# Optimization experiments

Measured on AMD Instinct MI355X. Metric: run time of the kernel, lower is better.

The kernel has to match this reference:

```python
import jax, jax.numpy as jnp
import numpy as np

N = 100_000   # nodes
E = 1_200_000 # edges
D = 64        # in_dim
H = 64        # hidden_dim
B = 1000      # graphs in batch
C = 10        # num_classes
TOPO = 64     # topo_dim
BN_EPS = 1e-5


def setup_inputs() -> dict:
    key = jax.random.key(0)
    ks = jax.random.split(key, 24)
    x = jax.random.normal(ks[0], (N, D), dtype=jnp.float32)
    edge_index = jax.random.randint(ks[1], (2, E), 0, N, dtype=jnp.int32)
    # sorted graph ids; force last id = B-1 so batch.max()+1 == B (matches torch path)
    batch = jnp.sort(jax.random.randint(ks[2], (N,), 0, B, dtype=jnp.int32)).at[-1].set(B - 1)
    topo = jax.random.normal(ks[3], (B, TOPO), dtype=jnp.float32)
    s = 0.05
    return {
        "x": x, "edge_index": edge_index, "batch": batch, "topo": topo,
        # conv1 MLP: Linear(D,H) -> BN(H) -> ReLU -> Linear(H,H) -> ReLU
        "W1a": jax.random.normal(ks[4], (D, H)) * s, "b1a": jax.random.normal(ks[5], (H,)) * s,
        "g1": 1.0 + jax.random.normal(ks[6], (H,)) * s, "be1": jax.random.normal(ks[7], (H,)) * s,
        "m1": jax.random.normal(ks[8], (H,)) * s, "v1": 0.5 + jax.random.uniform(ks[9], (H,)),
        "W1b": jax.random.normal(ks[10], (H, H)) * s, "b1b": jax.random.normal(ks[11], (H,)) * s,
        # conv2 MLP: Linear(H,H) -> BN(H) -> ReLU
        "W2": jax.random.normal(ks[12], (H, H)) * s, "b2": jax.random.normal(ks[13], (H,)) * s,
        "g2": 1.0 + jax.random.normal(ks[14], (H,)) * s, "be2": jax.random.normal(ks[15], (H,)) * s,
        "m2": jax.random.normal(ks[16], (H,)) * s, "v2": 0.5 + jax.random.uniform(ks[17], (H,)),
        # topo_net: Linear(TOPO,H) -> ReLU
        "Wt": jax.random.normal(ks[18], (TOPO, H)) * s, "bt": jax.random.normal(ks[19], (H,)) * s,
        # classifier: Linear(2H, C)
        "Wc": jax.random.normal(ks[20], (2 * H, C)) * s, "bc": jax.random.normal(ks[21], (C,)) * s,
    }


def _bn_eval(v, g, b, m, var):
    # BatchNorm1d in eval mode: affine with running stats
    return g * (v - m) * jax.lax.rsqrt(var + BN_EPS) + b


def _gin_agg(h, src, dst):
    # GINConv (eps=0): (1+eps)*x_i + sum_{j->i} x_j ; scatter-add over dst
    return h + jax.ops.segment_sum(h[src], dst, num_segments=N)


def reference(x, edge_index, batch, topo,
              W1a, b1a, g1, be1, m1, v1, W1b, b1b,
              W2, b2, g2, be2, m2, v2, Wt, bt, Wc, bc):
    src, dst = edge_index[0], edge_index[1]
    # conv1: MLP(agg(x)) = Lin -> BN -> ReLU -> Lin -> ReLU; outer relu from forward
    h = _gin_agg(x, src, dst)                              # [N, D]
    h = jax.nn.relu(_bn_eval(h @ W1a + b1a, g1, be1, m1, v1))
    h = jax.nn.relu(h @ W1b + b1b)                         # [N, H]
    h = jax.nn.relu(h)                                     # F.relu(conv1(...))
    # dropout(p=0.5) is identity in eval mode
    # conv2: Lin -> BN -> ReLU, then outer relu
    h = _gin_agg(h, src, dst)                              # [N, H]
    h = jax.nn.relu(_bn_eval(h @ W2 + b2, g2, be2, m2, v2))
    h = jax.nn.relu(h)
    # global_add_pool: sum nodes per graph
    x_struct = jax.ops.segment_sum(h, batch, num_segments=B)   # [B, H]
    # topo already [B, TOPO] => all reshape/pad branches are no-ops
    x_topo = jax.nn.relu(topo @ Wt + bt)                   # [B, H]
    combined = jnp.concatenate([x_struct, x_topo], axis=1) # [B, 2H]
    return combined @ Wc + bc                              # [B, C]
```

## Files before the change

### kernel.cpp

```cpp
#include <hip/hip_runtime.h>

#define N_NODES 100000
#define N_EDGES 1200000
#define DIM     64
#define BGRAPHS 1000
#define NCLASS  10
#define BN_EPS  1e-5f

#define NBUCK   256
#define NPB     391
#define MAGIC   10984572u
#define CHUNK   8192
#define NBLK_P  147
#define CAP     8192
#define NB_C    3125

typedef __attribute__((ext_vector_type(8))) short   bfx8;
typedef __attribute__((ext_vector_type(4))) float   f32x4;
typedef __attribute__((ext_vector_type(8))) unsigned short u16x8;

__device__ __forceinline__ unsigned short f2bf(float f) {
    unsigned u = __builtin_bit_cast(unsigned, f);
    unsigned r = (u + 0x7FFFu + ((u >> 16) & 1u)) >> 16;
    return (unsigned short)r;
}
__device__ __forceinline__ float bf2f(unsigned short h) {
    unsigned u = ((unsigned)h) << 16;
    return __builtin_bit_cast(float, u);
}

__global__ __launch_bounds__(256) void convhist_kernel(
    const float* __restrict__ x, unsigned short* __restrict__ xb,
    float* __restrict__ xs, const int* __restrict__ ei,
    int* __restrict__ gpart,
    const float* __restrict__ W1a, const float* __restrict__ W1b,
    const float* __restrict__ W2,
    unsigned short* __restrict__ w1ap, unsigned short* __restrict__ w1bp,
    unsigned short* __restrict__ w2p) {
    __shared__ int cnt[NBUCK];
    int t = threadIdx.x;
    if (blockIdx.x < NBLK_P) {
        int blk = blockIdx.x;
        cnt[t] = 0;
        __syncthreads();
        int e0 = blk * CHUNK;
        for (int i = t; i < CHUNK; i += 256) {
            int e = e0 + i;
            if (e >= N_EDGES) break;
            unsigned d = (unsigned)ei[N_EDGES + e];
            atomicAdd(&cnt[__umulhi(d, MAGIC)], 1);
        }
        __syncthreads();
        gpart[blk * NBUCK + t] = cnt[t];
    } else if (blockIdx.x < NBLK_P + NB_C) {
        int i = (blockIdx.x - NBLK_P) * 256 + t;
        const int n8 = N_NODES * DIM / 8;
        if (i < n8) {
            float4 a = ((const float4*)x)[i * 2];
            float4 b = ((const float4*)x)[i * 2 + 1];
            u16x8 o;
            o[0] = f2bf(a.x); o[1] = f2bf(a.y); o[2] = f2bf(a.z); o[3] = f2bf(a.w);
            o[4] = f2bf(b.x); o[5] = f2bf(b.y); o[6] = f2bf(b.z); o[7] = f2bf(b.w);
            ((u16x8*)xb)[i] = o;
        }
        if (i < BGRAPHS * DIM) xs[i] = 0.f;
    } else {
        const float* Ws[3] = {W1a, W1b, W2};
        unsigned short* Wp[3] = {w1ap, w1bp, w2p};
        #pragma unroll
        for (int wsel = 0; wsel < 3; ++wsel) {
            const float* W = Ws[wsel];
            #pragma unroll
            for (int r = 0; r < 2; ++r) {
                int e = r * 256 + t;
                int kt = e >> 8, q = (e >> 6) & 3, col = e & 63;
                u16x8 o;
                #pragma unroll
                for (int j = 0; j < 8; ++j)
                    o[j] = f2bf(W[(kt * 32 + q * 8 + j) * 64 + col]);
                ((u16x8*)Wp[wsel])[e] = o;
            }
        }
    }
}

__global__ __launch_bounds__(256) void scanB_kernel(const int* __restrict__ gpart,
                                                    int* __restrict__ base,
                                                    int* __restrict__ cursor) {
    __shared__ int tmp[256];
    int t = threadIdx.x;
    int s = 0;
    for (int blk = 0; blk < NBLK_P; ++blk) s += gpart[blk * NBUCK + t];
    tmp[t] = s;
    __syncthreads();
    for (int off = 1; off < 256; off <<= 1) {
        int a = (t >= off) ? tmp[t - off] : 0;
        __syncthreads();
        tmp[t] += a;
        __syncthreads();
    }
    int excl = tmp[t] - s;
    base[t] = excl;
    cursor[t] = excl;
    if (t == 255) base[256] = N_EDGES;
}

__global__ __launch_bounds__(256) void part_kernel(const int* __restrict__ ei,
                                                   int* __restrict__ cursor,
                                                   int* __restrict__ srcbuf,
                                                   unsigned short* __restrict__ dstlbuf) {
    __shared__ int cnt[NBUCK];
    __shared__ int cur[NBUCK];
    int t = threadIdx.x, blk = blockIdx.x;
    cnt[t] = 0;
    __syncthreads();
    int e0 = blk * CHUNK;
    for (int i = t; i < CHUNK; i += 256) {
        int e = e0 + i;
        if (e >= N_EDGES) break;
        unsigned d = (unsigned)ei[N_EDGES + e];
        atomicAdd(&cnt[__umulhi(d, MAGIC)], 1);
    }
    __syncthreads();
    cur[t] = atomicAdd(&cursor[t], cnt[t]);
    __syncthreads();
    for (int i = t; i < CHUNK; i += 256) {
        int e = e0 + i;
        if (e >= N_EDGES) break;
        unsigned d = (unsigned)ei[N_EDGES + e];
        int s = ei[e];
        int b = __umulhi(d, MAGIC);
        int pos = atomicAdd(&cur[b], 1);
        srcbuf[pos] = s;
        dstlbuf[pos] = (unsigned short)(d - b * NPB);
    }
}

__global__ __launch_bounds__(256) void refine_kernel(const int* __restrict__ srcbuf,
                                                     const unsigned short* __restrict__ dstlbuf,
                                                     const int* __restrict__ base,
                                                     int* __restrict__ csr_src,
                                                     int* __restrict__ rowptr) {
    __shared__ int cnt[NPB + 1];
    __shared__ int cur[NPB + 1];
    __shared__ int tmp[256];
    __shared__ int outb[CAP];
    int t = threadIdx.x, b = blockIdx.x;
    int beg = base[b];
    int end = base[b + 1];

    for (int i = t; i < NPB + 1; i += 256) cnt[i] = 0;
    __syncthreads();
    for (int i = beg + t; i < end; i += 256)
        atomicAdd(&cnt[dstlbuf[i]], 1);
    __syncthreads();

    int i0 = 2 * t, i1 = 2 * t + 1;
    int v0 = (i0 < NPB) ? cnt[i0] : 0;
    int v1 = (i1 < NPB) ? cnt[i1] : 0;
    int s = v0 + v1;
    tmp[t] = s;
    __syncthreads();
    for (int off = 1; off < 256; off <<= 1) {
        int a = (t >= off) ? tmp[t - off] : 0;
        __syncthreads();
        tmp[t] += a;
        __syncthreads();
    }
    int excl = tmp[t] - s;
    if (i0 < NPB) cur[i0] = excl;
    if (i1 < NPB) cur[i1] = excl + v0;
    {
        int g0 = b * NPB + i0;
        if (i0 < NPB && g0 < N_NODES) rowptr[g0] = beg + excl;
        int g1 = b * NPB + i1;
        if (i1 < NPB && g1 < N_NODES) rowptr[g1] = beg + excl + v0;
    }
    if (b == NBUCK - 1 && t == 0) rowptr[N_NODES] = N_EDGES;
    __syncthreads();

    for (int i = beg + t; i < end; i += 256) {
        int dl = dstlbuf[i];
        int pos = atomicAdd(&cur[dl], 1);
        if (pos < CAP) outb[pos] = srcbuf[i];
    }
    __syncthreads();

    int nb = end - beg; if (nb > CAP) nb = CAP;
    for (int i = t; i < nb; i += 256) csr_src[beg + i] = outb[i];
}

__global__ __launch_bounds__(256) void gather_kernel(const unsigned short* __restrict__ feat,
                                                     const int* __restrict__ rowptr,
                                                     const int* __restrict__ csr_src,
                                                     unsigned short* __restrict__ out) {
    int t = threadIdx.x;
    int node = blockIdx.x * 32 + (t >> 3);
    int q = t & 7;
    if (node >= N_NODES) return;
    const u16x8* f8 = (const u16x8*)feat;
    u16x8 sv = f8[(long long)node * 8 + q];
    float acc[8];
    #pragma unroll
    for (int j = 0; j < 8; ++j) acc[j] = bf2f(sv[j]);
    int beg = rowptr[node], end = rowptr[node + 1];
    int k = beg;
    int sn = (k < end) ? csr_src[k] : 0;
    while (k < end) {
        int sc = sn;
        ++k;
        if (k < end) sn = csr_src[k];
        u16x8 v = f8[(long long)sc * 8 + q];
        #pragma unroll
        for (int j = 0; j < 8; ++j) acc[j] += bf2f(v[j]);
    }
    u16x8 o;
    #pragma unroll
    for (int j = 0; j < 8; ++j) o[j] = f2bf(acc[j]);
    ((u16x8*)out)[(long long)node * 8 + q] = o;
}

__global__ __launch_bounds__(256) void mlp1_kernel(
    const unsigned short* __restrict__ h0,
    const unsigned short* __restrict__ w1ap, const float* __restrict__ b1a,
    const float* __restrict__ g1,  const float* __restrict__ be1,
    const float* __restrict__ m1,  const float* __restrict__ v1,
    const unsigned short* __restrict__ w1bp, const float* __restrict__ b1b,
    unsigned short* __restrict__ h2) {
    __shared__ unsigned short h1t[4][16 * 72];
    __shared__ unsigned short outt[4][16 * 64];

    int t = threadIdx.x;
    int w = t >> 6, lane = t & 63;
    int m = lane & 15, q = lane >> 4;
    int row0 = blockIdx.x * 64 + w * 16;

    const bfx8* wap = (const bfx8*)w1ap;
    const bfx8* wbp = (const bfx8*)w1bp;
    bfx8 wa[4][2], wb[4][2];
    #pragma unroll
    for (int nt = 0; nt < 4; ++nt) {
        #pragma unroll
        for (int kt = 0; kt < 2; ++kt) {
            int idx = (kt * 4 + q) * 64 + nt * 16 + m;
            wa[nt][kt] = wap[idx];
            wb[nt][kt] = wbp[idx];
        }
    }
    float A1[4], B1[4], B2c[4];
    #pragma unroll
    for (int nt = 0; nt < 4; ++nt) {
        int c = nt * 16 + m;
        float s = g1[c] * rsqrtf(v1[c] + BN_EPS);
        A1[nt] = s;
        B1[nt] = b1a[c] * s + (be1[c] - m1[c] * s);
        B2c[nt] = b1b[c];
    }

    int rowA = row0 + m;
    if (rowA > N_NODES - 1) rowA = N_NODES - 1;
    const bfx8* ap = (const bfx8*)(h0 + (long long)rowA * 64);
    bfx8 a0 = ap[q];
    bfx8 a1 = ap[4 + q];
    f32x4 acc[4];
    #pragma unroll
    for (int nt = 0; nt < 4; ++nt) {
        acc[nt] = (f32x4){0.f, 0.f, 0.f, 0.f};
        acc[nt] = __builtin_amdgcn_mfma_f32_16x16x32_bf16(a0, wa[nt][0], acc[nt], 0, 0, 0);
        acc[nt] = __builtin_amdgcn_mfma_f32_16x16x32_bf16(a1, wa[nt][1], acc[nt], 0, 0, 0);
    }
    #pragma unroll
    for (int nt = 0; nt < 4; ++nt)
        #pragma unroll
        for (int r = 0; r < 4; ++r) {
            float v = fmaxf(acc[nt][r] * A1[nt] + B1[nt], 0.f);
            h1t[w][(q * 4 + r) * 72 + nt * 16 + m] = f2bf(v);
        }
    __syncthreads();

    const bfx8* hp = (const bfx8*)&h1t[w][m * 72];
    bfx8 c0 = hp[q];
    bfx8 c1 = hp[4 + q];
    f32x4 acc2[4];
    #pragma unroll
    for (int nt = 0; nt < 4; ++nt) {
        acc2[nt] = (f32x4){0.f, 0.f, 0.f, 0.f};
        acc2[nt] = __builtin_amdgcn_mfma_f32_16x16x32_bf16(c0, wb[nt][0], acc2[nt], 0, 0, 0);
        acc2[nt] = __builtin_amdgcn_mfma_f32_16x16x32_bf16(c1, wb[nt][1], acc2[nt], 0, 0, 0);
    }
    #pragma unroll
    for (int nt = 0; nt < 4; ++nt)
        #pragma unroll
        for (int r = 0; r < 4; ++r) {
            float v = fmaxf(acc2[nt][r] + B2c[nt], 0.f);
            outt[w][(q * 4 + r) * 64 + nt * 16 + m] = f2bf(v);
        }
    __syncthreads();

    #pragma unroll
    for (int i = lane; i < 128; i += 64) {
        int rr = i >> 3, cc = i & 7;
        int rg = row0 + rr;
        if (rg < N_NODES)
            ((float4*)h2)[(long long)rg * 8 + cc] = *(const float4*)&outt[w][rr * 64 + cc * 8];
    }
}

__global__ __launch_bounds__(256) void mlp2_kernel(
    const unsigned short* __restrict__ h3,
    const unsigned short* __restrict__ w2p, const float* __restrict__ b2,
    const float* __restrict__ g2, const float* __restrict__ be2,
    const float* __restrict__ m2, const float* __restrict__ v2,
    const int* __restrict__ batch,
    float* __restrict__ xs) {
    __shared__ float pool[64 * 64];
    __shared__ int bts[64];

    int t = threadIdx.x;
    int w = t >> 6, lane = t & 63;
    int m = lane & 15, q = lane >> 4;
    int row0b = blockIdx.x * 64;
    int row0 = row0b + w * 16;

    const bfx8* wpp = (const bfx8*)w2p;
    bfx8 wf[4][2];
    #pragma unroll
    for (int nt = 0; nt < 4; ++nt)
        #pragma unroll
        for (int kt = 0; kt < 2; ++kt)
            wf[nt][kt] = wpp[(kt * 4 + q) * 64 + nt * 16 + m];
    float A[4], Bc[4];
    #pragma unroll
    for (int nt = 0; nt < 4; ++nt) {
        int c = nt * 16 + m;
        float s = g2[c] * rsqrtf(v2[c] + BN_EPS);
        A[nt] = s;
        Bc[nt] = b2[c] * s + (be2[c] - m2[c] * s);
    }
    if (t < 64) {
        int rg = row0b + t;
        bts[t] = (rg < N_NODES) ? batch[rg] : -1;
    }

    int rowA = row0 + m;
    if (rowA > N_NODES - 1) rowA = N_NODES - 1;
    const bfx8* ap = (const bfx8*)(h3 + (long long)rowA * 64);
    bfx8 a0 = ap[q];
    bfx8 a1 = ap[4 + q];
    f32x4 acc[4];
    #pragma unroll
    for (int nt = 0; nt < 4; ++nt) {
        acc[nt] = (f32x4){0.f, 0.f, 0.f, 0.f};
        acc[nt] = __builtin_amdgcn_mfma_f32_16x16x32_bf16(a0, wf[nt][0], acc[nt], 0, 0, 0);
        acc[nt] = __builtin_amdgcn_mfma_f32_16x16x32_bf16(a1, wf[nt][1], acc[nt], 0, 0, 0);
    }
    #pragma unroll
    for (int nt = 0; nt < 4; ++nt)
        #pragma unroll
        for (int r = 0; r < 4; ++r) {
            float v = fmaxf(acc[nt][r] * A[nt] + Bc[nt], 0.f);
            pool[(w * 16 + q * 4 + r) * 64 + nt * 16 + m] = v;
        }
    __syncthreads();

    int col = t & 63;
    int r0 = (t >> 6) * 16;
    int cb = bts[r0];
    float cur = 0.f;
    #pragma unroll
    for (int r = 0; r < 16; ++r) {
        int b = bts[r0 + r];
        if (b != cb) {
            if (cb >= 0) unsafeAtomicAdd(&xs[cb * 64 + col], cur);
            cb = b;
            cur = 0.f;
        }
        cur += pool[(r0 + r) * 64 + col];
    }
    if (cb >= 0) unsafeAtomicAdd(&xs[cb * 64 + col], cur);
}

__global__ __launch_bounds__(64) void head_kernel(
    const float* __restrict__ xs, const float* __restrict__ topo,
    const float* __restrict__ Wt, const float* __restrict__ bt,
    const float* __restrict__ Wc, const float* __restrict__ bc,
    float* __restrict__ out) {
    __shared__ float trow[64];
    __shared__ float comb[128];
    int b = blockIdx.x;
    int h = threadIdx.x;
    trow[h] = topo[b * 64 + h];
    __syncthreads();
    float acc = bt[h];
    #pragma unroll
    for (int k = 0; k < 64; ++k) acc += trow[k] * Wt[k * 64 + h];
    comb[h] = xs[b * 64 + h];
    comb[64 + h] = fmaxf(acc, 0.f);
    __syncthreads();
    if (h < NCLASS) {
        float o = bc[h];
        #pragma unroll
        for (int k = 0; k < 128; ++k) o += comb[k] * Wc[k * NCLASS + h];
        out[b * NCLASS + h] = o;
    }
}

extern "C" void kernel_launch(void* const* d_in, const int* in_sizes, int n_in,
                              void* d_out, int out_size, void* d_ws, size_t ws_size,
                              hipStream_t stream) {
    const float* x     = (const float*)d_in[0];
    const int*   ei    = (const int*)d_in[1];
    const int*   batch = (const int*)d_in[2];
    const float* topo  = (const float*)d_in[3];
    const float* W1a   = (const float*)d_in[4];
    const float* b1a   = (const float*)d_in[5];
    const float* g1    = (const float*)d_in[6];
    const float* be1   = (const float*)d_in[7];
    const float* m1    = (const float*)d_in[8];
    const float* v1    = (const float*)d_in[9];
    const float* W1b   = (const float*)d_in[10];
    const float* b1b   = (const float*)d_in[11];
    const float* W2    = (const float*)d_in[12];
    const float* b2    = (const float*)d_in[13];
    const float* g2    = (const float*)d_in[14];
    const float* be2   = (const float*)d_in[15];
    const float* m2    = (const float*)d_in[16];
    const float* v2    = (const float*)d_in[17];
    const float* Wt    = (const float*)d_in[18];
    const float* bt    = (const float*)d_in[19];
    const float* Wc    = (const float*)d_in[20];
    const float* bc    = (const float*)d_in[21];
    float* out = (float*)d_out;

    char* p = (char*)d_ws;
    unsigned short* xbf  = (unsigned short*)p; p += (size_t)N_NODES * DIM * 2;
    unsigned short* bufA = (unsigned short*)p; p += (size_t)N_NODES * DIM * 2;
    unsigned short* bufB = (unsigned short*)p; p += (size_t)N_NODES * DIM * 2;
    float* xs      = (float*)p; p += (size_t)BGRAPHS * DIM * 4;
    int*   rowptr  = (int*)p;   p += (size_t)(N_NODES + 16) * 4;
    int*   gpart   = (int*)p;   p += (size_t)NBLK_P * NBUCK * 4;
    int*   base    = (int*)p;   p += 1040;
    int*   cursor  = (int*)p;   p += 1024;
    unsigned short* w1ap = (unsigned short*)p; p += 512 * 16;
    unsigned short* w1bp = (unsigned short*)p; p += 512 * 16;
    unsigned short* w2p  = (unsigned short*)p; p += 512 * 16;
    int*   srcbuf  = (int*)p;   p += (size_t)N_EDGES * 4;
    unsigned short* dstlbuf = (unsigned short*)p; p += (size_t)N_EDGES * 2;
    int*   csr_src = (int*)p;

    convhist_kernel<<<NBLK_P + NB_C + 1, 256, 0, stream>>>(
        x, xbf, xs, ei, gpart, W1a, W1b, W2, w1ap, w1bp, w2p);
    scanB_kernel<<<1, 256, 0, stream>>>(gpart, base, cursor);
    part_kernel<<<NBLK_P, 256, 0, stream>>>(ei, cursor, srcbuf, dstlbuf);
    refine_kernel<<<NBUCK, 256, 0, stream>>>(srcbuf, dstlbuf, base, csr_src, rowptr);
    gather_kernel<<<(N_NODES + 31) / 32, 256, 0, stream>>>(xbf, rowptr, csr_src, bufA);
    mlp1_kernel<<<(N_NODES + 63) / 64, 256, 0, stream>>>(
        bufA, w1ap, b1a, g1, be1, m1, v1, w1bp, b1b, bufB);
    gather_kernel<<<(N_NODES + 31) / 32, 256, 0, stream>>>(bufB, rowptr, csr_src, bufA);
    mlp2_kernel<<<(N_NODES + 63) / 64, 256, 0, stream>>>(
        bufA, w2p, b2, g2, be2, m2, v2, batch, xs);
    head_kernel<<<BGRAPHS, 64, 0, stream>>>(xs, topo, Wt, bt, Wc, bc, out);
}
```

Baseline: 246.9 us.

## Apply linear layers before aggregation and fuse BN/ReLU and pooling into gathers

Uses linearity of the GIN sum: x@W1a is computed in the prep kernel before aggregation, and h@W2 in the mid MLP, so the gather kernels run on projected features and apply the folded BN affine plus ReLU in their epilogue. The second gather also does the global add pool directly, which removes the separate mlp2 kernel and one full feature round-trip. BN scale and shift are precomputed once into a small buffer, and part_kernel reuses the histogram counts instead of recounting. Rounding changes because the projection is rounded to bf16 before summation, and the guards for node counts that are not a multiple of 32 are dropped.

```diff
diff --git a/kernel.cpp b/kernel.cpp
--- a/kernel.cpp
+++ b/kernel.cpp
@@ -13,7 +13,7 @@
 #define CHUNK   8192
 #define NBLK_P  147
 #define CAP     8192
-#define NB_C    3125
+#define NB_G    1563
 
 typedef __attribute__((ext_vector_type(8))) short   bfx8;
 typedef __attribute__((ext_vector_type(4))) float   f32x4;
@@ -29,15 +29,30 @@
     return __builtin_bit_cast(float, u);
 }
 
-__global__ __launch_bounds__(256) void convhist_kernel(
-    const float* __restrict__ x, unsigned short* __restrict__ xb,
-    float* __restrict__ xs, const int* __restrict__ ei,
+__device__ __forceinline__ bfx8 load_wfrag(const float* __restrict__ W, int kt, int q, int col) {
+    bfx8 f;
+    #pragma unroll
+    for (int j = 0; j < 8; ++j)
+        f[j] = (short)f2bf(W[(kt * 32 + q * 8 + j) * 64 + col]);
+    return f;
+}
+
+__global__ __launch_bounds__(256) void prep_kernel(
+    const float* __restrict__ x, const int* __restrict__ ei,
     int* __restrict__ gpart,
-    const float* __restrict__ W1a, const float* __restrict__ W1b,
-    const float* __restrict__ W2,
-    unsigned short* __restrict__ w1ap, unsigned short* __restrict__ w1bp,
-    unsigned short* __restrict__ w2p) {
+    const float* __restrict__ W1a, unsigned short* __restrict__ y0,
+    float* __restrict__ xs,
+    const float* __restrict__ W1b, const float* __restrict__ W2,
+    unsigned short* __restrict__ w1bp, unsigned short* __restrict__ w2p,
+    const float* __restrict__ b1a, const float* __restrict__ g1,
+    const float* __restrict__ be1, const float* __restrict__ m1,
+    const float* __restrict__ v1,
+    const float* __restrict__ b2,  const float* __restrict__ g2,
+    const float* __restrict__ be2, const float* __restrict__ m2,
+    const float* __restrict__ v2,
+    float* __restrict__ AB) {
     __shared__ int cnt[NBUCK];
+    __shared__ unsigned short outt[4][16 * 64];
     int t = threadIdx.x;
     if (blockIdx.x < NBLK_P) {
         int blk = blockIdx.x;
@@ -52,23 +67,54 @@
         }
         __syncthreads();
         gpart[blk * NBUCK + t] = cnt[t];
-    } else if (blockIdx.x < NBLK_P + NB_C) {
-        int i = (blockIdx.x - NBLK_P) * 256 + t;
-        const int n8 = N_NODES * DIM / 8;
-        if (i < n8) {
-            float4 a = ((const float4*)x)[i * 2];
-            float4 b = ((const float4*)x)[i * 2 + 1];
-            u16x8 o;
-            o[0] = f2bf(a.x); o[1] = f2bf(a.y); o[2] = f2bf(a.z); o[3] = f2bf(a.w);
-            o[4] = f2bf(b.x); o[5] = f2bf(b.y); o[6] = f2bf(b.z); o[7] = f2bf(b.w);
-            ((u16x8*)xb)[i] = o;
-        }
-        if (i < BGRAPHS * DIM) xs[i] = 0.f;
+    } else if (blockIdx.x < NBLK_P + NB_G) {
+        int g = blockIdx.x - NBLK_P;
+        if (g < (BGRAPHS * DIM) / 256) xs[g * 256 + t] = 0.f;
+        int w = t >> 6, lane = t & 63;
+        int m = lane & 15, q = lane >> 4;
+        int row0 = g * 64 + w * 16;
+
+        bfx8 wa[4][2];
+        #pragma unroll
+        for (int nt = 0; nt < 4; ++nt)
+            #pragma unroll
+            for (int kt = 0; kt < 2; ++kt)
+                wa[nt][kt] = load_wfrag(W1a, kt, q, nt * 16 + m);
+
+        int rowA = row0 + m;
+        if (rowA > N_NODES - 1) rowA = N_NODES - 1;
+        const float* xp = x + (long long)rowA * 64;
+        bfx8 a0, a1;
+        #pragma unroll
+        for (int j = 0; j < 8; ++j) {
+            a0[j] = (short)f2bf(xp[q * 8 + j]);
+            a1[j] = (short)f2bf(xp[32 + q * 8 + j]);
+        }
+        f32x4 acc[4];
+        #pragma unroll
+        for (int nt = 0; nt < 4; ++nt) {
+            acc[nt] = (f32x4){0.f, 0.f, 0.f, 0.f};
+            acc[nt] = __builtin_amdgcn_mfma_f32_16x16x32_bf16(a0, wa[nt][0], acc[nt], 0, 0, 0);
+            acc[nt] = __builtin_amdgcn_mfma_f32_16x16x32_bf16(a1, wa[nt][1], acc[nt], 0, 0, 0);
+        }
+        #pragma unroll
+        for (int nt = 0; nt < 4; ++nt)
+            #pragma unroll
+            for (int r = 0; r < 4; ++r)
+                outt[w][(q * 4 + r) * 64 + nt * 16 + m] = f2bf(acc[nt][r]);
+        __syncthreads();
+        #pragma unroll
+        for (int i = lane; i < 128; i += 64) {
+            int rr = i >> 3, cc = i & 7;
+            int rg = row0 + rr;
+            if (rg < N_NODES)
+                ((float4*)y0)[(long long)rg * 8 + cc] = *(const float4*)&outt[w][rr * 64 + cc * 8];
+        }
     } else {
-        const float* Ws[3] = {W1a, W1b, W2};
-        unsigned short* Wp[3] = {w1ap, w1bp, w2p};
-        #pragma unroll
-        for (int wsel = 0; wsel < 3; ++wsel) {
+        const float* Ws[2] = {W1b, W2};
+        unsigned short* Wp[2] = {w1bp, w2p};
+        #pragma unroll
+        for (int wsel = 0; wsel < 2; ++wsel) {
             const float* W = Ws[wsel];
             #pragma unroll
             for (int r = 0; r < 2; ++r) {
@@ -81,6 +127,14 @@
                 ((u16x8*)Wp[wsel])[e] = o;
             }
         }
+        if (t < 64) {
+            float s1 = g1[t] * rsqrtf(v1[t] + BN_EPS);
+            AB[t]       = s1;
+            AB[64 + t]  = b1a[t] * s1 + (be1[t] - m1[t] * s1);
+            float s2 = g2[t] * rsqrtf(v2[t] + BN_EPS);
+            AB[128 + t] = s2;
+            AB[192 + t] = b2[t] * s2 + (be2[t] - m2[t] * s2);
+        }
     }
 }
 
@@ -106,24 +160,15 @@
 }
 
 __global__ __launch_bounds__(256) void part_kernel(const int* __restrict__ ei,
+                                                   const int* __restrict__ gpart,
                                                    int* __restrict__ cursor,
                                                    int* __restrict__ srcbuf,
                                                    unsigned short* __restrict__ dstlbuf) {
-    __shared__ int cnt[NBUCK];
     __shared__ int cur[NBUCK];
     int t = threadIdx.x, blk = blockIdx.x;
-    cnt[t] = 0;
+    cur[t] = atomicAdd(&cursor[t], gpart[blk * NBUCK + t]);
     __syncthreads();
     int e0 = blk * CHUNK;
-    for (int i = t; i < CHUNK; i += 256) {
-        int e = e0 + i;
-        if (e >= N_EDGES) break;
-        unsigned d = (unsigned)ei[N_EDGES + e];
-        atomicAdd(&cnt[__umulhi(d, MAGIC)], 1);
-    }
-    __syncthreads();
-    cur[t] = atomicAdd(&cursor[t], cnt[t]);
-    __syncthreads();
     for (int i = t; i < CHUNK; i += 256) {
         int e = e0 + i;
         if (e >= N_EDGES) break;
@@ -190,14 +235,14 @@
     for (int i = t; i < nb; i += 256) csr_src[beg + i] = outb[i];
 }
 
-__global__ __launch_bounds__(256) void gather_kernel(const unsigned short* __restrict__ feat,
-                                                     const int* __restrict__ rowptr,
-                                                     const int* __restrict__ csr_src,
-                                                     unsigned short* __restrict__ out) {
+__global__ __launch_bounds__(256) void gather_bn1_kernel(
+    const unsigned short* __restrict__ feat,
+    const int* __restrict__ rowptr, const int* __restrict__ csr_src,
+    const float* __restrict__ AB,
+    unsigned short* __restrict__ out) {
     int t = threadIdx.x;
     int node = blockIdx.x * 32 + (t >> 3);
     int q = t & 7;
-    if (node >= N_NODES) return;
     const u16x8* f8 = (const u16x8*)feat;
     u16x8 sv = f8[(long long)node * 8 + q];
     float acc[8];
@@ -216,18 +261,19 @@
     }
     u16x8 o;
     #pragma unroll
-    for (int j = 0; j < 8; ++j) o[j] = f2bf(acc[j]);
+    for (int j = 0; j < 8; ++j) {
+        int c = q * 8 + j;
+        o[j] = f2bf(fmaxf(acc[j] * AB[c] + AB[64 + c], 0.f));
+    }
     ((u16x8*)out)[(long long)node * 8 + q] = o;
 }
 
-__global__ __launch_bounds__(256) void mlp1_kernel(
-    const unsigned short* __restrict__ h0,
-    const unsigned short* __restrict__ w1ap, const float* __restrict__ b1a,
-    const float* __restrict__ g1,  const float* __restrict__ be1,
-    const float* __restrict__ m1,  const float* __restrict__ v1,
+__global__ __launch_bounds__(256) void mlpmid_kernel(
+    const unsigned short* __restrict__ h1,
     const unsigned short* __restrict__ w1bp, const float* __restrict__ b1b,
-    unsigned short* __restrict__ h2) {
-    __shared__ unsigned short h1t[4][16 * 72];
+    const unsigned short* __restrict__ w2p,
+    unsigned short* __restrict__ y2) {
+    __shared__ unsigned short h2t[4][16 * 72];
     __shared__ unsigned short outt[4][16 * 64];
 
     int t = threadIdx.x;
@@ -235,66 +281,57 @@
     int m = lane & 15, q = lane >> 4;
     int row0 = blockIdx.x * 64 + w * 16;
 
-    const bfx8* wap = (const bfx8*)w1ap;
     const bfx8* wbp = (const bfx8*)w1bp;
-    bfx8 wa[4][2], wb[4][2];
-    #pragma unroll
-    for (int nt = 0; nt < 4; ++nt) {
+    const bfx8* wcp = (const bfx8*)w2p;
+    bfx8 wb[4][2], wc[4][2];
+    #pragma unroll
+    for (int nt = 0; nt < 4; ++nt)
         #pragma unroll
         for (int kt = 0; kt < 2; ++kt) {
             int idx = (kt * 4 + q) * 64 + nt * 16 + m;
-            wa[nt][kt] = wap[idx];
             wb[nt][kt] = wbp[idx];
-        }
-    }
-    float A1[4], B1[4], B2c[4];
-    #pragma unroll
-    for (int nt = 0; nt < 4; ++nt) {
-        int c = nt * 16 + m;
-        float s = g1[c] * rsqrtf(v1[c] + BN_EPS);
-        A1[nt] = s;
-        B1[nt] = b1a[c] * s + (be1[c] - m1[c] * s);
-        B2c[nt] = b1b[c];
-    }
+            wc[nt][kt] = wcp[idx];
+        }
+    float B1b[4];
+    #pragma unroll
+    for (int nt = 0; nt < 4; ++nt) B1b[nt] = b1b[nt * 16 + m];
 
     int rowA = row0 + m;
     if (rowA > N_NODES - 1) rowA = N_NODES - 1;
-    const bfx8* ap = (const bfx8*)(h0 + (long long)rowA * 64);
+    const bfx8* ap = (const bfx8*)(h1 + (long long)rowA * 64);
     bfx8 a0 = ap[q];
     bfx8 a1 = ap[4 + q];
     f32x4 acc[4];
     #pragma unroll
     for (int nt = 0; nt < 4; ++nt) {
         acc[nt] = (f32x4){0.f, 0.f, 0.f, 0.f};
-        acc[nt] = __builtin_amdgcn_mfma_f32_16x16x32_bf16(a0, wa[nt][0], acc[nt], 0, 0, 0);
-        acc[nt] = __builtin_amdgcn_mfma_f32_16x16x32_bf16(a1, wa[nt][1], acc[nt], 0, 0, 0);
+        acc[nt] = __builtin_amdgcn_mfma_f32_16x16x32_bf16(a0, wb[nt][0], acc[nt], 0, 0, 0);
+        acc[nt] = __builtin_amdgcn_mfma_f32_16x16x32_bf16(a1, wb[nt][1], acc[nt], 0, 0, 0);
     }
     #pragma unroll
     for (int nt = 0; nt < 4; ++nt)
         #pragma unroll
         for (int r = 0; r < 4; ++r) {
-            float v = fmaxf(acc[nt][r] * A1[nt] + B1[nt], 0.f);
-            h1t[w][(q * 4 + r) * 72 + nt * 16 + m] = f2bf(v);
-        }
-    __syncthreads();
-
-    const bfx8* hp = (const bfx8*)&h1t[w][m * 72];
+            float v = fmaxf(acc[nt][r] + B1b[nt], 0.f);
+            h2t[w][(q * 4 + r) * 72 + nt * 16 + m] = f2bf(v);
+        }
+    __syncthreads();
+
+    const bfx8* hp = (const bfx8*)&h2t[w][m * 72];
     bfx8 c0 = hp[q];
     bfx8 c1 = hp[4 + q];
     f32x4 acc2[4];
     #pragma unroll
     for (int nt = 0; nt < 4; ++nt) {
         acc2[nt] = (f32x4){0.f, 0.f, 0.f, 0.f};
-        acc2[nt] = __builtin_amdgcn_mfma_f32_16x16x32_bf16(c0, wb[nt][0], acc2[nt], 0, 0, 0);
-        acc2[nt] = __builtin_amdgcn_mfma_f32_16x16x32_bf16(c1, wb[nt][1], acc2[nt], 0, 0, 0);
+        acc2[nt] = __builtin_amdgcn_mfma_f32_16x16x32_bf16(c0, wc[nt][0], acc2[nt], 0, 0, 0);
+        acc2[nt] = __builtin_amdgcn_mfma_f32_16x16x32_bf16(c1, wc[nt][1], acc2[nt], 0, 0, 0);
     }
     #pragma unroll
     for (int nt = 0; nt < 4; ++nt)
         #pragma unroll
-        for (int r = 0; r < 4; ++r) {
-            float v = fmaxf(acc2[nt][r] + B2c[nt], 0.f);
-            outt[w][(q * 4 + r) * 64 + nt * 16 + m] = f2bf(v);
-        }
+        for (int r = 0; r < 4; ++r)
+            outt[w][(q * 4 + r) * 64 + nt * 16 + m] = f2bf(acc2[nt][r]);
     __syncthreads();
 
     #pragma unroll
@@ -302,82 +339,60 @@
         int rr = i >> 3, cc = i & 7;
         int rg = row0 + rr;
         if (rg < N_NODES)
-            ((float4*)h2)[(long long)rg * 8 + cc] = *(const float4*)&outt[w][rr * 64 + cc * 8];
-    }
-}
-
-__global__ __launch_bounds__(256) void mlp2_kernel(
-    const unsigned short* __restrict__ h3,
-    const unsigned short* __restrict__ w2p, const float* __restrict__ b2,
-    const float* __restrict__ g2, const float* __restrict__ be2,
-    const float* __restrict__ m2, const float* __restrict__ v2,
-    const int* __restrict__ batch,
+            ((float4*)y2)[(long long)rg * 8 + cc] = *(const float4*)&outt[w][rr * 64 + cc * 8];
+    }
+}
+
+__global__ __launch_bounds__(256) void gather_pool_kernel(
+    const unsigned short* __restrict__ feat,
+    const int* __restrict__ rowptr, const int* __restrict__ csr_src,
+    const float* __restrict__ AB, const int* __restrict__ batch,
     float* __restrict__ xs) {
-    __shared__ float pool[64 * 64];
-    __shared__ int bts[64];
-
+    __shared__ float h4[32 * 65];
+    __shared__ int bts[32];
     int t = threadIdx.x;
-    int w = t >> 6, lane = t & 63;
-    int m = lane & 15, q = lane >> 4;
-    int row0b = blockIdx.x * 64;
-    int row0 = row0b + w * 16;
-
-    const bfx8* wpp = (const bfx8*)w2p;
-    bfx8 wf[4][2];
-    #pragma unroll
-    for (int nt = 0; nt < 4; ++nt)
-        #pragma unroll
-        for (int kt = 0; kt < 2; ++kt)
-            wf[nt][kt] = wpp[(kt * 4 + q) * 64 + nt * 16 + m];
-    float A[4], Bc[4];
-    #pragma unroll
-    for (int nt = 0; nt < 4; ++nt) {
-        int c = nt * 16 + m;
-        float s = g2[c] * rsqrtf(v2[c] + BN_EPS);
-        A[nt] = s;
-        Bc[nt] = b2[c] * s + (be2[c] - m2[c] * s);
-    }
-    if (t < 64) {
-        int rg = row0b + t;
-        bts[t] = (rg < N_NODES) ? batch[rg] : -1;
-    }
-
-    int rowA = row0 + m;
-    if (rowA > N_NODES - 1) rowA = N_NODES - 1;
-    const bfx8* ap = (const bfx8*)(h3 + (long long)rowA * 64);
-    bfx8 a0 = ap[q];
-    bfx8 a1 = ap[4 + q];
-    f32x4 acc[4];
-    #pragma unroll
-    for (int nt = 0; nt < 4; ++nt) {
-        acc[nt] = (f32x4){0.f, 0.f, 0.f, 0.f};
-        acc[nt] = __builtin_amdgcn_mfma_f32_16x16x32_bf16(a0, wf[nt][0], acc[nt], 0, 0, 0);
-        acc[nt] = __builtin_amdgcn_mfma_f32_16x16x32_bf16(a1, wf[nt][1], acc[nt], 0, 0, 0);
-    }
-    #pragma unroll
-    for (int nt = 0; nt < 4; ++nt)
-        #pragma unroll
-        for (int r = 0; r < 4; ++r) {
-            float v = fmaxf(acc[nt][r] * A[nt] + Bc[nt], 0.f);
-            pool[(w * 16 + q * 4 + r) * 64 + nt * 16 + m] = v;
-        }
+    int nl = t >> 3;
+    int q = t & 7;
+    int node = blockIdx.x * 32 + nl;
+    if (t < 32) bts[t] = batch[blockIdx.x * 32 + t];
+    const u16x8* f8 = (const u16x8*)feat;
+    u16x8 sv = f8[(long long)node * 8 + q];
+    float acc[8];
+    #pragma unroll
+    for (int j = 0; j < 8; ++j) acc[j] = bf2f(sv[j]);
+    int beg = rowptr[node], end = rowptr[node + 1];
+    int k = beg;
+    int sn = (k < end) ? csr_src[k] : 0;
+    while (k < end) {
+        int sc = sn;
+        ++k;
+        if (k < end) sn = csr_src[k];
+        u16x8 v = f8[(long long)sc * 8 + q];
+        #pragma unroll
+        for (int j = 0; j < 8; ++j) acc[j] += bf2f(v[j]);
+    }
+    #pragma unroll
+    for (int j = 0; j < 8; ++j) {
+        int c = q * 8 + j;
+        h4[nl * 65 + c] = fmaxf(acc[j] * AB[128 + c] + AB[192 + c], 0.f);
+    }
     __syncthreads();
 
     int col = t & 63;
-    int r0 = (t >> 6) * 16;
+    int r0 = (t >> 6) * 8;
     int cb = bts[r0];
     float cur = 0.f;
     #pragma unroll
-    for (int r = 0; r < 16; ++r) {
+    for (int r = 0; r < 8; ++r) {
         int b = bts[r0 + r];
         if (b != cb) {
-            if (cb >= 0) unsafeAtomicAdd(&xs[cb * 64 + col], cur);
+            unsafeAtomicAdd(&xs[cb * 64 + col], cur);
             cb = b;
             cur = 0.f;
         }
-        cur += pool[(r0 + r) * 64 + col];
-    }
-    if (cb >= 0) unsafeAtomicAdd(&xs[cb * 64 + col], cur);
+        cur += h4[(r0 + r) * 65 + col];
+    }
+    unsafeAtomicAdd(&xs[cb * 64 + col], cur);
 }
 
 __global__ __launch_bounds__(64) void head_kernel(
@@ -433,31 +448,29 @@
     float* out = (float*)d_out;
 
     char* p = (char*)d_ws;
-    unsigned short* xbf  = (unsigned short*)p; p += (size_t)N_NODES * DIM * 2;
-    unsigned short* bufA = (unsigned short*)p; p += (size_t)N_NODES * DIM * 2;
-    unsigned short* bufB = (unsigned short*)p; p += (size_t)N_NODES * DIM * 2;
+    unsigned short* y0   = (unsigned short*)p; p += (size_t)N_NODES * DIM * 2;
+    unsigned short* h1b  = (unsigned short*)p; p += (size_t)N_NODES * DIM * 2;
+    unsigned short* y2b  = (unsigned short*)p; p += (size_t)N_NODES * DIM * 2;
     float* xs      = (float*)p; p += (size_t)BGRAPHS * DIM * 4;
     int*   rowptr  = (int*)p;   p += (size_t)(N_NODES + 16) * 4;
     int*   gpart   = (int*)p;   p += (size_t)NBLK_P * NBUCK * 4;
     int*   base    = (int*)p;   p += 1040;
     int*   cursor  = (int*)p;   p += 1024;
-    unsigned short* w1ap = (unsigned short*)p; p += 512 * 16;
     unsigned short* w1bp = (unsigned short*)p; p += 512 * 16;
     unsigned short* w2p  = (unsigned short*)p; p += 512 * 16;
+    float* AB      = (float*)p; p += 256 * 4;
     int*   srcbuf  = (int*)p;   p += (size_t)N_EDGES * 4;
     unsigned short* dstlbuf = (unsigned short*)p; p += (size_t)N_EDGES * 2;
     int*   csr_src = (int*)p;
 
-    convhist_kernel<<<NBLK_P + NB_C + 1, 256, 0, stream>>>(
-        x, xbf, xs, ei, gpart, W1a, W1b, W2, w1ap, w1bp, w2p);
+    prep_kernel<<<NBLK_P + NB_G + 1, 256, 0, stream>>>(
+        x, ei, gpart, W1a, y0, xs, W1b, W2, w1bp, w2p,
+        b1a, g1, be1, m1, v1, b2, g2, be2, m2, v2, AB);
     scanB_kernel<<<1, 256, 0, stream>>>(gpart, base, cursor);
-    part_kernel<<<NBLK_P, 256, 0, stream>>>(ei, cursor, srcbuf, dstlbuf);
+    part_kernel<<<NBLK_P, 256, 0, stream>>>(ei, gpart, cursor, srcbuf, dstlbuf);
     refine_kernel<<<NBUCK, 256, 0, stream>>>(srcbuf, dstlbuf, base, csr_src, rowptr);
-    gather_kernel<<<(N_NODES + 31) / 32, 256, 0, stream>>>(xbf, rowptr, csr_src, bufA);
-    mlp1_kernel<<<(N_NODES + 63) / 64, 256, 0, stream>>>(
-        bufA, w1ap, b1a, g1, be1, m1, v1, w1bp, b1b, bufB);
-    gather_kernel<<<(N_NODES + 31) / 32, 256, 0, stream>>>(bufB, rowptr, csr_src, bufA);
-    mlp2_kernel<<<(N_NODES + 63) / 64, 256, 0, stream>>>(
-        bufA, w2p, b2, g2, be2, m2, v2, batch, xs);
+    gather_bn1_kernel<<<N_NODES / 32, 256, 0, stream>>>(y0, rowptr, csr_src, AB, h1b);
+    mlpmid_kernel<<<(N_NODES + 63) / 64, 256, 0, stream>>>(h1b, w1bp, b1b, w2p, y2b);
+    gather_pool_kernel<<<N_NODES / 32, 256, 0, stream>>>(y2b, rowptr, csr_src, AB, batch, xs);
     head_kernel<<<BGRAPHS, 64, 0, stream>>>(xs, topo, Wt, bt, Wc, bc, out);
 }
```

After: 238.3 us. 1.04x faster.
